# Kernel optimization log

Hardware: AMD Instinct MI355X
Metric: run time of the kernel (lower is better)

Reference implementation:

```python
import jax, jax.numpy as jnp
import numpy as np

B, N, C_IN, C_COORD, K = 2, 8192, 64, 3, 16
C_CAT = C_IN + C_COORD  # 67
HID1, HID2, C_OUT = 32, 64, 64


def setup_inputs() -> dict:
    key = jax.random.key(0)
    ks = jax.random.split(key, 10)
    s = 0.05
    return {
        "point_features": jax.random.normal(ks[0], (B, N, C_IN), jnp.float32),
        "coords": jax.random.uniform(ks[1], (B, N, C_COORD), jnp.float32),
        "w1": jax.random.normal(ks[2], (HID1, C_CAT), jnp.float32) * s,
        "b1": jax.random.normal(ks[3], (HID1,), jnp.float32) * s,
        "w2": jax.random.normal(ks[4], (HID2, HID1), jnp.float32) * s,
        "b2": jax.random.normal(ks[5], (HID2,), jnp.float32) * s,
        "w3": jax.random.normal(ks[6], (C_OUT, HID2), jnp.float32) * s,
        "b3": jax.random.normal(ks[7], (C_OUT,), jnp.float32) * s,
        "aggr_w": jax.random.normal(ks[8], (K,), jnp.float32) * s,
        "aggr_b": jax.random.normal(ks[9], (1,), jnp.float32) * s,
    }


def _knn_idx(coords):
    # squared pairwise distances: [B, N, N]
    sq = jnp.sum(coords * coords, axis=-1)
    d2 = sq[:, :, None] + sq[:, None, :] - 2.0 * jnp.einsum("bnc,bmc->bnm", coords, coords)
    # k smallest distances -> top_k of negated; self (d=0) lands at slot 0
    _, idx = jax.lax.top_k(-d2, K)  # [B, N, K]
    return idx


def reference(point_features, coords, w1, b1, w2, b2, w3, b3, aggr_w, aggr_b):
    idx = _knn_idx(coords)  # [B, N, K] int32
    feats = jnp.concatenate([point_features, coords], axis=-1)  # [B, N, C_CAT]
    # gather neighbor features -> [B, N, K, C_CAT]
    g = jax.vmap(lambda f, i: f[i])(feats, idx)
    # relative coords w.r.t. neighbor 0 (self)
    rel = g[..., -C_COORD:] - g[:, :, 0:1, -C_COORD:]
    g = jnp.concatenate([g[..., :C_IN], rel], axis=-1)
    # point pooling: max over K of raw input-feature channels
    y_pool = jnp.max(g[..., :C_IN], axis=2)  # [B, N, C_IN]
    # kernel MLP: stacked 1x1 convs, NO activations (act_func=None in source)
    h = jnp.einsum("bnkc,oc->bnko", g, w1) + b1
    h = jnp.einsum("bnkc,oc->bnko", h, w2) + b2
    h = jnp.einsum("bnkc,oc->bnko", h, w3) + b3  # [B, N, K, C_OUT]
    # attentive aggregation: Conv2d(K, 1, 1) over the K axis
    y_aggr = jnp.einsum("bnko,k->bno", h, aggr_w) + aggr_b  # [B, N, C_OUT]
    out_sum = jnp.sum(h, axis=2)  # [B, N, C_OUT]
    # concat order matches torch: (sum, pool, aggr), then permute -> B x N x C'
    return jnp.concatenate([out_sum, y_pool, y_aggr], axis=-1)
```

## Files before the change

### kernel.cpp

```cpp
#include <hip/hip_runtime.h>
#include <stdint.h>


typedef unsigned short u16;
typedef unsigned int   u32;
typedef unsigned long long u64;

#define NPTS  8192
#define KNB   16
#define SCAP  128
#define CAPA  512
#define QPW   8

__device__ __forceinline__ float bf2f(u16 u) {
    union { u32 i; float f; } v; v.i = ((u32)u) << 16; return v.f;
}
__device__ __forceinline__ u16 f2bf(float f) {
    u32 x = __float_as_uint(f);
    return (u16)((x + 0x7FFFu + ((x >> 16) & 1u)) >> 16);
}
__device__ __forceinline__ u32 fordkey(float f) {
    u32 u = __float_as_uint(f);
    return u ^ ((u32)((int)u >> 31) | 0x80000000u);
}
__device__ __forceinline__ u64 shflxor64(u64 v, int m) {
    int lo = __shfl_xor((int)(u32)v, m, 64);
    int hi = __shfl_xor((int)(u32)(v >> 32), m, 64);
    return ((u64)(u32)hi << 32) | (u32)lo;
}
__device__ __forceinline__ void wave_fence() {
    asm volatile("s_waitcnt lgkmcnt(0)" ::: "memory");
    __builtin_amdgcn_sched_barrier(0);
}
__device__ __forceinline__ float sq_np32(float x, float y, float z) {
    return __fadd_rn(__fadd_rn(__fmul_rn(x, x), __fmul_rn(y, y)), __fmul_rn(z, z));
}
__device__ __forceinline__ float d2_ref(float qx, float qy, float qz, float qsq,
                                        float x, float y, float z, float sq) {
    float dot = fmaf(z, qz, fmaf(y, qy, __fmul_rn(x, qx)));
    return __fsub_rn(__fadd_rn(qsq, sq), __fmul_rn(2.0f, dot));
}
__device__ __forceinline__ int cellof(float v) {
    int c = (int)floorf(v * 8.0f);
    return c < 0 ? 0 : (c > 7 ? 7 : c);
}

__global__ __launch_bounds__(256) void pack_count_kernel(
    const float* __restrict__ pf, const float* __restrict__ coords,
    u16* __restrict__ pfh, int* __restrict__ counts) {
    int gid = blockIdx.x * 256 + threadIdx.x;
    pfh[gid] = f2bf(pf[gid]);
    if (gid < 2 * NPTS) {
        float x = coords[gid * 3 + 0];
        float y = coords[gid * 3 + 1];
        float z = coords[gid * 3 + 2];
        int b = gid >> 13;
        int cell = (cellof(x) * 8 + cellof(y)) * 8 + cellof(z);
        atomicAdd(&counts[b * 512 + cell], 1);
    }
}

__global__ __launch_bounds__(512) void scan_kernel(
    const int* __restrict__ counts, int* __restrict__ cellStart,
    int* __restrict__ cellOffset) {
    __shared__ int s[512];
    int b = blockIdx.x, t = threadIdx.x;
    int myc = counts[b * 512 + t];
    s[t] = myc; __syncthreads();
#pragma unroll
    for (int off = 1; off < 512; off <<= 1) {
        int v = (t >= off) ? s[t - off] : 0; __syncthreads();
        s[t] += v; __syncthreads();
    }
    int excl = s[t] - myc;
    cellStart[b * 513 + t] = excl;
    cellOffset[b * 512 + t] = excl;
    if (t == 511) cellStart[b * 513 + 512] = s[511];
}

__global__ __launch_bounds__(256) void scatter_kernel(
    const float* __restrict__ coords, int* __restrict__ cellOffset,
    float4* __restrict__ spts, int* __restrict__ sidx) {
    int gid = blockIdx.x * 256 + threadIdx.x;
    float x = coords[gid * 3 + 0];
    float y = coords[gid * 3 + 1];
    float z = coords[gid * 3 + 2];
    int b = gid >> 13, i = gid & (NPTS - 1);
    int cell = (cellof(x) * 8 + cellof(y)) * 8 + cellof(z);
    int pos = atomicAdd(&cellOffset[b * 512 + cell], 1);
    spts[b * NPTS + pos] = make_float4(x, y, z, sq_np32(x, y, z));
    sidx[b * NPTS + pos] = i;
}

__device__ __forceinline__ void scan_seg(
    const float4* __restrict__ sp, const int* __restrict__ cs,
    u64* __restrict__ surv, int base, int z0, int z1,
    float qx, float qy, float qz, float qsq, float tau, int lane, int& cnt) {
    if (z0 > z1) return;
    int s = cs[base + z0], e = cs[base + z1 + 1];
    for (int i0 = s; i0 < e; i0 += 64) {
        int i = i0 + lane;
        bool valid = (i < e);
        int ii = valid ? i : (e - 1);
        float4 c = sp[ii];
        float d2 = d2_ref(qx, qy, qz, qsq, c.x, c.y, c.z, c.w);
        bool pass = valid && (d2 <= tau);
        u64 mask = __ballot(pass);
        if (pass) {
            int pre = __builtin_amdgcn_mbcnt_hi((u32)(mask >> 32),
                      __builtin_amdgcn_mbcnt_lo((u32)mask, 0));
            int pos = cnt + pre;
            if (pos < SCAP)
                surv[pos] = ((u64)fordkey(d2) << 32) | (u32)ii;
        }
        cnt += (int)__popcll(mask);
    }
}

__global__ __launch_bounds__(256, 6) void knn_kernel(
    const float4* __restrict__ spts, const int* __restrict__ sidx,
    const int* __restrict__ cellStart, int* __restrict__ idx_out) {
    __shared__ u64 allk_s[4][CAPA];
    __shared__ u64 surv_s[4][SCAP];

    const int lane = threadIdx.x & 63;
    const int wid  = threadIdx.x >> 6;
    u64* __restrict__ allk = allk_s[wid];
    u64* __restrict__ surv = surv_s[wid];

    const int blk  = blockIdx.x;
    const int sblk = (blk & 7) * 512 + (blk >> 3);
    const int p    = sblk * 4 + wid;
    const int b    = p >> 13;
    const float4* sp = spts + b * NPTS;
    const int*    si = sidx + b * NPTS;
    const int*    cs = cellStart + b * 513;

    float4 qc = sp[p & (NPTS - 1)];
    const float qx = qc.x, qy = qc.y, qz = qc.z, qsq = qc.w;
    int cqx = cellof(qx), cqy = cellof(qy), cqz = cellof(qz);

    const int ucqx = __builtin_amdgcn_readfirstlane(cqx);
    const int ucqy = __builtin_amdgcn_readfirstlane(cqy);
    const int ucqz = __builtin_amdgcn_readfirstlane(cqz);

    const int ax0 = max(ucqx - 1, 0), ax1 = min(ucqx + 1, 7);
    const int ay0 = max(ucqy - 1, 0), ay1 = min(ucqy + 1, 7);
    const int az0 = max(ucqz - 1, 0), az1 = min(ucqz + 1, 7);

    int segS[9], segE[9];
#pragma unroll
    for (int u = 0; u < 9; ++u) {
        int cx = ucqx - 1 + (u / 3);
        int cy = ucqy - 1 + (u % 3);
        bool ok = (cx >= 0) && (cx <= 7) && (cy >= 0) && (cy <= 7);
        if (ok) {
            int base = (cx * 8 + cy) * 8;
            segS[u] = cs[base + az0];
            segE[u] = cs[base + az1 + 1];
        } else {
            segS[u] = 0;
            segE[u] = 0;
        }
    }

    float dmin = 3.0e38f;
    int cnt0 = 0;
    bool ovf = false;
#pragma unroll
    for (int u = 0; u < 9; ++u) {
        int s = segS[u], e = segE[u];
#pragma unroll 1
        for (int i0 = s; i0 < e; i0 += 64) {
            int i = i0 + lane;
            bool valid = (i < e);
            int ii = valid ? i : (e - 1);
            float4 c = sp[ii];
            float d2 = d2_ref(qx, qy, qz, qsq, c.x, c.y, c.z, c.w);
            if (valid) dmin = fminf(dmin, d2);
            int add = (e - i0 < 64) ? (e - i0) : 64;
            if (!ovf && cnt0 + add <= CAPA) {
                if (valid)
                    allk[cnt0 + lane] = ((u64)fordkey(d2) << 32) | (u32)ii;
                cnt0 += add;
            } else {
                ovf = true;
            }
        }
    }
    wave_fence();

    {
        float v = dmin;
#pragma unroll
        for (int k = 2; k <= 64; k <<= 1) {
#pragma unroll
            for (int j2 = k >> 1; j2 >= 1; j2 >>= 1) {
                float o = __shfl_xor(v, j2, 64);
                bool lo = (lane & j2) == 0;
                bool up = (lane & k) == 0;
                float mn = fminf(v, o), mx = fmaxf(v, o);
                v = (lo == up) ? mn : mx;
            }
        }
        dmin = __shfl(v, 15, 64);
    }
    const float tau = dmin;

    float rr = sqrtf(tau + 1e-5f) + 1e-6f;
    int bx0 = max((int)floorf((qx - rr) * 8.0f), 0);
    int bx1 = min((int)floorf((qx + rr) * 8.0f), 7);
    int by0 = max((int)floorf((qy - rr) * 8.0f), 0);
    int by1 = min((int)floorf((qy + rr) * 8.0f), 7);
    int bz0 = max((int)floorf((qz - rr) * 8.0f), 0);
    int bz1 = min((int)floorf((qz + rr) * 8.0f), 7);
    int cnt = 0;
    if (!ovf) {
        const u32 taukey = fordkey(tau);
        for (int i0 = 0; i0 < cnt0; i0 += 64) {
            int i = i0 + lane;
            bool valid = (i < cnt0);
            u64 kk = valid ? allk[i] : ~0ull;
            bool pass = valid && ((u32)(kk >> 32) <= taukey);
            u64 mask = __ballot(pass);
            if (pass) {
                int pre = __builtin_amdgcn_mbcnt_hi((u32)(mask >> 32),
                          __builtin_amdgcn_mbcnt_lo((u32)mask, 0));
                int pos = cnt + pre;
                if (pos < SCAP) surv[pos] = kk;
            }
            cnt += (int)__popcll(mask);
        }
    }
#pragma unroll 1
    for (int cx = bx0; cx <= bx1; ++cx)
#pragma unroll 1
        for (int cy = by0; cy <= by1; ++cy) {
            int base = (cx * 8 + cy) * 8;
            bool colInA = !ovf && cx >= ax0 && cx <= ax1 &&
                          cy >= ay0 && cy <= ay1;
            if (colInA) {
                scan_seg(sp, cs, surv, base, bz0, min(az0 - 1, bz1),
                         qx, qy, qz, qsq, tau, lane, cnt);
                scan_seg(sp, cs, surv, base, max(az1 + 1, bz0), bz1,
                         qx, qy, qz, qsq, tau, lane, cnt);
            } else {
                scan_seg(sp, cs, surv, base, bz0, bz1,
                         qx, qy, qz, qsq, tau, lane, cnt);
            }
        }
    wave_fence();

    int myidx = 0;
    if (cnt <= 64) {
        u32 k32 = 0xffffffffu, p32 = 0xffffffffu;
        if (lane < cnt) {
            u64 kk = surv[lane];
            k32 = (u32)(kk >> 32);
            p32 = (u32)kk;
        }
#pragma unroll
        for (int k = 2; k <= 64; k <<= 1) {
#pragma unroll
            for (int j2 = k >> 1; j2 >= 1; j2 >>= 1) {
                u32 ok = (u32)__shfl_xor((int)k32, j2, 64);
                u32 op = (u32)__shfl_xor((int)p32, j2, 64);
                bool lo = (lane & j2) == 0;
                bool up = (lane & k) == 0;
                bool takemin = (lo == up);
                bool less = (ok < k32) || (ok == k32 && op < p32);
                bool take = (less == takemin);
                k32 = take ? ok : k32;
                p32 = take ? op : p32;
            }
        }
        myidx = (int)p32;
    } else {
        int cc = cnt > SCAP ? SCAP : cnt;
        u64 a0 = (lane < cc) ? surv[lane] : ~0ull;
        u64 a1 = (64 + lane < cc) ? surv[64 + lane] : ~0ull;
        if (a1 < a0) { u64 tmp = a0; a0 = a1; a1 = tmp; }
#pragma unroll 1
        for (int r = 0; r < 16; ++r) {
            u64 m = a0;
#pragma unroll
            for (int d = 1; d < 64; d <<= 1) {
                u64 o = shflxor64(m, d);
                m = (o < m) ? o : m;
            }
            if (a0 == m) { a0 = a1; a1 = ~0ull; }
            if (lane == r) myidx = (int)(u32)(m & 0xffffffffu);
        }
    }
    if (lane < KNB) {
        const int q = si[p & (NPTS - 1)];
        idx_out[((size_t)b * NPTS + q) * KNB + lane] =
            si[myidx & (NPTS - 1)];
    }
}

__global__ __launch_bounds__(64) void mlp_kernel(
    const u16* __restrict__ pfh, const float* __restrict__ coords,
    const float* __restrict__ w1, const float* __restrict__ b1,
    const float* __restrict__ w2, const float* __restrict__ b2,
    const float* __restrict__ w3, const float* __restrict__ b3,
    const float* __restrict__ aw, const float* __restrict__ ab,
    const int* __restrict__ knn_idx, const int* __restrict__ sidx,
    float* __restrict__ out) {

    __shared__ __attribute__((aligned(16))) float vbuf[2][68];
    __shared__ __attribute__((aligned(16))) float h1buf[2][36];

    const int lane = threadIdx.x;
    const int r    = lane & 31;
    const int vec  = lane >> 5;

    float w1r[68];
#pragma unroll
    for (int c = 0; c < 67; ++c) w1r[c] = w1[r * 67 + c];
    w1r[67] = 0.0f;
    float w2r[32];
    {
        const float4* p = (const float4*)(w2 + lane * 32);
#pragma unroll
        for (int c4 = 0; c4 < 8; ++c4) {
            float4 v = p[c4];
            w2r[c4 * 4 + 0] = v.x; w2r[c4 * 4 + 1] = v.y;
            w2r[c4 * 4 + 2] = v.z; w2r[c4 * 4 + 3] = v.w;
        }
    }
    float w3r[64];
    {
        const float4* p = (const float4*)(w3 + lane * 64);
#pragma unroll
        for (int c4 = 0; c4 < 16; ++c4) {
            float4 v = p[c4];
            w3r[c4 * 4 + 0] = v.x; w3r[c4 * 4 + 1] = v.y;
            w3r[c4 * 4 + 2] = v.z; w3r[c4 * 4 + 3] = v.w;
        }
    }
    float awr[16];
#pragma unroll
    for (int k = 0; k < 16; ++k) awr[k] = aw[k];
    float sa = 0.0f;
#pragma unroll
    for (int k = 0; k < 16; ++k) sa += awr[k];
    const float b1v = b1[r], b2v = b2[lane], b3v = b3[lane], abv = ab[0];
    const float c1 = (vec == 0) ? 16.0f : sa;

    const int sblk = (blockIdx.x & 7) * 256 + (blockIdx.x >> 3);

#pragma unroll 1
    for (int t = 0; t < QPW; ++t) {
        const int gp = sblk * QPW + t;
        const int b  = gp >> 13;
        const int q  = sidx[(size_t)b * NPTS + (gp & (NPTS - 1))];
        const int gq = b * NPTS + q;
        const u16*   pfb = pfh + (size_t)b * NPTS * 64;
        const float* cb  = coords + (size_t)b * NPTS * 3;

        int myi = knn_idx[(size_t)gq * KNB + (lane & 15)] & (NPTS - 1);

        float pool = -3.0e38f, G1 = 0.0f, Ga = 0.0f;
#pragma unroll
        for (int k = 0; k < 16; ++k) {
            int nk = __shfl(myi, k, 64);
            float v = bf2f(pfb[nk * 64 + lane]);
            pool = fmaxf(pool, v);
            G1 += v;
            Ga = fmaf(awr[k], v, Ga);
        }
        vbuf[0][lane] = G1;
        vbuf[1][lane] = Ga;

        if (lane < 48) {
            int j  = lane >> 4;
            int i0 = __shfl(myi, 0, 64);
            float rel  = cb[myi * 3 + j] - cb[i0 * 3 + j];
            float wrel = awr[lane & 15] * rel;
#pragma unroll
            for (int d = 1; d < 16; d <<= 1) {
                rel  += __shfl_xor(rel, d, 64);
                wrel += __shfl_xor(wrel, d, 64);
            }
            if ((lane & 15) == 0) { vbuf[0][64 + j] = rel; vbuf[1][64 + j] = wrel; }
        }
        if (lane == 0) { vbuf[0][67] = 0.0f; vbuf[1][67] = 0.0f; }
        __syncthreads();

        float acc = c1 * b1v;
        {
            const float4* vp = (const float4*)(&vbuf[vec][0]);
#pragma unroll
            for (int c4 = 0; c4 < 17; ++c4) {
                float4 g4 = vp[c4];
                acc = fmaf(g4.x, w1r[c4 * 4 + 0], acc);
                acc = fmaf(g4.y, w1r[c4 * 4 + 1], acc);
                acc = fmaf(g4.z, w1r[c4 * 4 + 2], acc);
                acc = fmaf(g4.w, w1r[c4 * 4 + 3], acc);
            }
        }
        h1buf[vec][r] = acc;
        __syncthreads();

        float a0 = 16.0f * b2v, a1 = sa * b2v;
        {
            const float4* p0 = (const float4*)(&h1buf[0][0]);
            const float4* p1 = (const float4*)(&h1buf[1][0]);
#pragma unroll
            for (int c4 = 0; c4 < 8; ++c4) {
                float4 x0 = p0[c4], x1 = p1[c4];
                a0 = fmaf(x0.x, w2r[c4 * 4 + 0], a0);
                a0 = fmaf(x0.y, w2r[c4 * 4 + 1], a0);
                a0 = fmaf(x0.z, w2r[c4 * 4 + 2], a0);
                a0 = fmaf(x0.w, w2r[c4 * 4 + 3], a0);
                a1 = fmaf(x1.x, w2r[c4 * 4 + 0], a1);
                a1 = fmaf(x1.y, w2r[c4 * 4 + 1], a1);
                a1 = fmaf(x1.z, w2r[c4 * 4 + 2], a1);
                a1 = fmaf(x1.w, w2r[c4 * 4 + 3], a1);
            }
        }
        __syncthreads();
        vbuf[0][lane] = a0;
        vbuf[1][lane] = a1;
        __syncthreads();

        float s1 = 16.0f * b3v, sA = sa * b3v;
        {
            const float4* p0 = (const float4*)(&vbuf[0][0]);
            const float4* p1 = (const float4*)(&vbuf[1][0]);
#pragma unroll
            for (int c4 = 0; c4 < 16; ++c4) {
                float4 x0 = p0[c4], x1 = p1[c4];
                s1 = fmaf(x0.x, w3r[c4 * 4 + 0], s1);
                s1 = fmaf(x0.y, w3r[c4 * 4 + 1], s1);
                s1 = fmaf(x0.z, w3r[c4 * 4 + 2], s1);
                s1 = fmaf(x0.w, w3r[c4 * 4 + 3], s1);
                sA = fmaf(x1.x, w3r[c4 * 4 + 0], sA);
                sA = fmaf(x1.y, w3r[c4 * 4 + 1], sA);
                sA = fmaf(x1.z, w3r[c4 * 4 + 2], sA);
                sA = fmaf(x1.w, w3r[c4 * 4 + 3], sA);
            }
        }
        float* op = out + (size_t)gq * 192;
        op[lane]       = s1;
        op[64 + lane]  = pool;
        op[128 + lane] = sA + abv;
        __syncthreads();
    }
}

extern "C" void kernel_launch(void* const* d_in, const int* in_sizes, int n_in,
                              void* d_out, int out_size, void* d_ws, size_t ws_size,
                              hipStream_t stream) {
    const float* pf     = (const float*)d_in[0];
    const float* coords = (const float*)d_in[1];
    const float* w1     = (const float*)d_in[2];
    const float* b1     = (const float*)d_in[3];
    const float* w2     = (const float*)d_in[4];
    const float* b2     = (const float*)d_in[5];
    const float* w3     = (const float*)d_in[6];
    const float* b3     = (const float*)d_in[7];
    const float* aw     = (const float*)d_in[8];
    const float* ab     = (const float*)d_in[9];

    char* ws = (char*)d_ws;
    int*    knn_idx    = (int*)ws;
    u16*    pfh        = (u16*)(ws + (1 << 20));
    float4* spts       = (float4*)(ws + (3 << 20));
    int*    sidx       = (int*)(ws + (3 << 20) + (256 << 10));
    int*    cellStart  = (int*)(ws + (3 << 20) + (320 << 10));
    int*    counts     = (int*)(ws + (3 << 20) + (328 << 10));
    int*    cellOffset = (int*)(ws + (3 << 20) + (336 << 10));
    float*  outp       = (float*)d_out;

    hipMemsetAsync(counts, 0, 2 * 512 * sizeof(int), stream);
    pack_count_kernel<<<4096, 256, 0, stream>>>(pf, coords, pfh, counts);
    scan_kernel<<<2, 512, 0, stream>>>(counts, cellStart, cellOffset);
    scatter_kernel<<<64, 256, 0, stream>>>(coords, cellOffset, spts, sidx);
    knn_kernel<<<4096, 256, 0, stream>>>(spts, sidx, cellStart, knn_idx);
    mlp_kernel<<<2048, 64, 0, stream>>>(pfh, coords, w1, b1, w2, b2, w3, b3,
                                        aw, ab, knn_idx, sidx, outp);
}
```

Before: 141.4 us.

## Process two KNN queries per wave with compact u32 candidate keys

Each wave now handles two query points, interleaving their candidate passes, bitonic threshold reductions and final sorts so the independent shuffle and load chains can overlap and hide latency. Candidate storage in LDS shrinks from 64-bit key/index pairs to 32-bit keys, with the index rebuilt from per-segment prefix offsets during filtering. Overflow is now decided up front from segment totals against a smaller capacity. The grid is halved to match. The trade-offs are higher register pressure and LDS use per wave, and a wave now waits on whichever of its two queries is slower.

```diff
diff --git a/kernel.cpp b/kernel.cpp
--- a/kernel.cpp
+++ b/kernel.cpp
@@ -9,7 +9,7 @@
 #define NPTS  8192
 #define KNB   16
 #define SCAP  128
-#define CAPA  512
+#define CAPA  480
 #define QPW   8
 
 __device__ __forceinline__ float bf2f(u16 u) {
@@ -117,59 +117,36 @@
     }
 }
 
-__global__ __launch_bounds__(256, 6) void knn_kernel(
-    const float4* __restrict__ spts, const int* __restrict__ sidx,
-    const int* __restrict__ cellStart, int* __restrict__ idx_out) {
-    __shared__ u64 allk_s[4][CAPA];
-    __shared__ u64 surv_s[4][SCAP];
-
-    const int lane = threadIdx.x & 63;
-    const int wid  = threadIdx.x >> 6;
-    u64* __restrict__ allk = allk_s[wid];
-    u64* __restrict__ surv = surv_s[wid];
-
-    const int blk  = blockIdx.x;
-    const int sblk = (blk & 7) * 512 + (blk >> 3);
-    const int p    = sblk * 4 + wid;
-    const int b    = p >> 13;
-    const float4* sp = spts + b * NPTS;
-    const int*    si = sidx + b * NPTS;
-    const int*    cs = cellStart + b * 513;
-
-    float4 qc = sp[p & (NPTS - 1)];
-    const float qx = qc.x, qy = qc.y, qz = qc.z, qsq = qc.w;
-    int cqx = cellof(qx), cqy = cellof(qy), cqz = cellof(qz);
-
-    const int ucqx = __builtin_amdgcn_readfirstlane(cqx);
-    const int ucqy = __builtin_amdgcn_readfirstlane(cqy);
-    const int ucqz = __builtin_amdgcn_readfirstlane(cqz);
-
-    const int ax0 = max(ucqx - 1, 0), ax1 = min(ucqx + 1, 7);
-    const int ay0 = max(ucqy - 1, 0), ay1 = min(ucqy + 1, 7);
-    const int az0 = max(ucqz - 1, 0), az1 = min(ucqz + 1, 7);
-
-    int segS[9], segE[9];
+__device__ __forceinline__ void segtab(
+    const int* __restrict__ cs, int ucx, int ucy, int az0, int az1,
+    int* segS, int* segE, int* pre, int& cnt0) {
+    int run = 0;
 #pragma unroll
     for (int u = 0; u < 9; ++u) {
-        int cx = ucqx - 1 + (u / 3);
-        int cy = ucqy - 1 + (u % 3);
+        int cx = ucx - 1 + (u / 3);
+        int cy = ucy - 1 + (u % 3);
         bool ok = (cx >= 0) && (cx <= 7) && (cy >= 0) && (cy <= 7);
+        int s = 0, e = 0;
         if (ok) {
             int base = (cx * 8 + cy) * 8;
-            segS[u] = cs[base + az0];
-            segE[u] = cs[base + az1 + 1];
-        } else {
-            segS[u] = 0;
-            segE[u] = 0;
-        }
-    }
-
-    float dmin = 3.0e38f;
-    int cnt0 = 0;
-    bool ovf = false;
+            s = cs[base + az0];
+            e = cs[base + az1 + 1];
+        }
+        segS[u] = s; segE[u] = e; pre[u] = run;
+        run += e - s;
+    }
+    cnt0 = run;
+}
+
+__device__ __forceinline__ void passA_one(
+    const float4* __restrict__ sp, u32* __restrict__ allk, int lane,
+    float qx, float qy, float qz, float qsq,
+    const int* segS, const int* segE, const int* pre, bool ovf,
+    float& dmin) {
 #pragma unroll
     for (int u = 0; u < 9; ++u) {
         int s = segS[u], e = segE[u];
+        int cb = pre[u] - s;
 #pragma unroll 1
         for (int i0 = s; i0 < e; i0 += 64) {
             int i = i0 + lane;
@@ -177,36 +154,46 @@
             int ii = valid ? i : (e - 1);
             float4 c = sp[ii];
             float d2 = d2_ref(qx, qy, qz, qsq, c.x, c.y, c.z, c.w);
-            if (valid) dmin = fminf(dmin, d2);
-            int add = (e - i0 < 64) ? (e - i0) : 64;
-            if (!ovf && cnt0 + add <= CAPA) {
-                if (valid)
-                    allk[cnt0 + lane] = ((u64)fordkey(d2) << 32) | (u32)ii;
-                cnt0 += add;
-            } else {
-                ovf = true;
-            }
-        }
-    }
-    wave_fence();
-
-    {
-        float v = dmin;
-#pragma unroll
-        for (int k = 2; k <= 64; k <<= 1) {
-#pragma unroll
-            for (int j2 = k >> 1; j2 >= 1; j2 >>= 1) {
-                float o = __shfl_xor(v, j2, 64);
-                bool lo = (lane & j2) == 0;
-                bool up = (lane & k) == 0;
-                float mn = fminf(v, o), mx = fmaxf(v, o);
-                v = (lo == up) ? mn : mx;
-            }
-        }
-        dmin = __shfl(v, 15, 64);
-    }
-    const float tau = dmin;
-
+            if (valid) {
+                dmin = fminf(dmin, d2);
+                if (!ovf) allk[cb + i] = fordkey(d2);
+            }
+        }
+    }
+}
+
+__device__ __forceinline__ int filter_lds(
+    const u32* __restrict__ allk, u64* __restrict__ surv,
+    const int* segS, const int* pre, int cnt0, u32 taukey, int lane) {
+    int cnt = 0;
+    for (int i0 = 0; i0 < cnt0; i0 += 64) {
+        int j = i0 + lane;
+        bool valid = (j < cnt0);
+        u32 kk = valid ? allk[j] : 0xffffffffu;
+        bool pass = valid && (kk <= taukey);
+        int off = segS[0];
+#pragma unroll
+        for (int u = 1; u < 9; ++u)
+            off = (j >= pre[u]) ? (segS[u] - pre[u]) : off;
+        int ii = j + off;
+        u64 mask = __ballot(pass);
+        if (pass) {
+            int pc = __builtin_amdgcn_mbcnt_hi((u32)(mask >> 32),
+                     __builtin_amdgcn_mbcnt_lo((u32)mask, 0));
+            int pos = cnt + pc;
+            if (pos < SCAP) surv[pos] = ((u64)kk << 32) | (u32)ii;
+        }
+        cnt += (int)__popcll(mask);
+    }
+    return cnt;
+}
+
+__device__ __forceinline__ void bbox_scan(
+    const float4* __restrict__ sp, const int* __restrict__ cs,
+    u64* __restrict__ surv,
+    float qx, float qy, float qz, float qsq, float tau,
+    int ax0, int ax1, int ay0, int ay1, int az0, int az1, bool ovf,
+    int lane, int& cnt) {
     float rr = sqrtf(tau + 1e-5f) + 1e-6f;
     int bx0 = max((int)floorf((qx - rr) * 8.0f), 0);
     int bx1 = min((int)floorf((qx + rr) * 8.0f), 7);
@@ -214,24 +201,6 @@
     int by1 = min((int)floorf((qy + rr) * 8.0f), 7);
     int bz0 = max((int)floorf((qz - rr) * 8.0f), 0);
     int bz1 = min((int)floorf((qz + rr) * 8.0f), 7);
-    int cnt = 0;
-    if (!ovf) {
-        const u32 taukey = fordkey(tau);
-        for (int i0 = 0; i0 < cnt0; i0 += 64) {
-            int i = i0 + lane;
-            bool valid = (i < cnt0);
-            u64 kk = valid ? allk[i] : ~0ull;
-            bool pass = valid && ((u32)(kk >> 32) <= taukey);
-            u64 mask = __ballot(pass);
-            if (pass) {
-                int pre = __builtin_amdgcn_mbcnt_hi((u32)(mask >> 32),
-                          __builtin_amdgcn_mbcnt_lo((u32)mask, 0));
-                int pos = cnt + pre;
-                if (pos < SCAP) surv[pos] = kk;
-            }
-            cnt += (int)__popcll(mask);
-        }
-    }
 #pragma unroll 1
     for (int cx = bx0; cx <= bx1; ++cx)
 #pragma unroll 1
@@ -249,8 +218,10 @@
                          qx, qy, qz, qsq, tau, lane, cnt);
             }
         }
-    wave_fence();
-
+}
+
+__device__ __forceinline__ int sel_one(const u64* __restrict__ surv,
+                                       int cnt, int lane) {
     int myidx = 0;
     if (cnt <= 64) {
         u32 k32 = 0xffffffffu, p32 = 0xffffffffu;
@@ -292,10 +263,132 @@
             if (lane == r) myidx = (int)(u32)(m & 0xffffffffu);
         }
     }
+    return myidx;
+}
+
+__global__ __launch_bounds__(256, 6) void knn_kernel(
+    const float4* __restrict__ spts, const int* __restrict__ sidx,
+    const int* __restrict__ cellStart, int* __restrict__ idx_out) {
+    __shared__ u32 allk_s[4][2][CAPA];
+    __shared__ u64 surv_s[4][2][SCAP];
+
+    const int lane = threadIdx.x & 63;
+    const int wid  = threadIdx.x >> 6;
+    u32* __restrict__ allkA = allk_s[wid][0];
+    u32* __restrict__ allkB = allk_s[wid][1];
+    u64* __restrict__ survA = surv_s[wid][0];
+    u64* __restrict__ survB = surv_s[wid][1];
+
+    const int blk  = blockIdx.x;
+    const int sblk = (blk & 7) * 256 + (blk >> 3);
+    const int pg   = sblk * 8 + wid * 2;
+    const int b    = pg >> 13;
+    const float4* sp = spts + b * NPTS;
+    const int*    si = sidx + b * NPTS;
+    const int*    cs = cellStart + b * 513;
+    const int plA = pg & (NPTS - 1);
+    const int plB = plA + 1;
+
+    float4 qcA = sp[plA];
+    float4 qcB = sp[plB];
+    const float qxA = qcA.x, qyA = qcA.y, qzA = qcA.z, qsA = qcA.w;
+    const float qxB = qcB.x, qyB = qcB.y, qzB = qcB.z, qsB = qcB.w;
+
+    const int uxA = __builtin_amdgcn_readfirstlane(cellof(qxA));
+    const int uyA = __builtin_amdgcn_readfirstlane(cellof(qyA));
+    const int uzA = __builtin_amdgcn_readfirstlane(cellof(qzA));
+    const int uxB = __builtin_amdgcn_readfirstlane(cellof(qxB));
+    const int uyB = __builtin_amdgcn_readfirstlane(cellof(qyB));
+    const int uzB = __builtin_amdgcn_readfirstlane(cellof(qzB));
+
+    const int axA0 = max(uxA - 1, 0), axA1 = min(uxA + 1, 7);
+    const int ayA0 = max(uyA - 1, 0), ayA1 = min(uyA + 1, 7);
+    const int azA0 = max(uzA - 1, 0), azA1 = min(uzA + 1, 7);
+    const int axB0 = max(uxB - 1, 0), axB1 = min(uxB + 1, 7);
+    const int ayB0 = max(uyB - 1, 0), ayB1 = min(uyB + 1, 7);
+    const int azB0 = max(uzB - 1, 0), azB1 = min(uzB + 1, 7);
+
+    int segSA[9], segEA[9], preA[9], cnt0A;
+    int segSB[9], segEB[9], preB[9], cnt0B;
+    segtab(cs, uxA, uyA, azA0, azA1, segSA, segEA, preA, cnt0A);
+    segtab(cs, uxB, uyB, azB0, azB1, segSB, segEB, preB, cnt0B);
+    const bool ovfA = cnt0A > CAPA;
+    const bool ovfB = cnt0B > CAPA;
+
+    float dminA = 3.0e38f, dminB = 3.0e38f;
+    passA_one(sp, allkA, lane, qxA, qyA, qzA, qsA, segSA, segEA, preA, ovfA, dminA);
+    passA_one(sp, allkB, lane, qxB, qyB, qzB, qsB, segSB, segEB, preB, ovfB, dminB);
+    wave_fence();
+
+    float vA = dminA, vB = dminB;
+#pragma unroll
+    for (int k = 2; k <= 64; k <<= 1) {
+#pragma unroll
+        for (int j2 = k >> 1; j2 >= 1; j2 >>= 1) {
+            float oA = __shfl_xor(vA, j2, 64);
+            float oB = __shfl_xor(vB, j2, 64);
+            bool lo = (lane & j2) == 0;
+            bool up = (lane & k) == 0;
+            bool tm = (lo == up);
+            float mnA = fminf(vA, oA), mxA = fmaxf(vA, oA);
+            float mnB = fminf(vB, oB), mxB = fmaxf(vB, oB);
+            vA = tm ? mnA : mxA;
+            vB = tm ? mnB : mxB;
+        }
+    }
+    const float tauA = __shfl(vA, 15, 64);
+    const float tauB = __shfl(vB, 15, 64);
+
+    int cntA = 0, cntB = 0;
+    if (!ovfA) cntA = filter_lds(allkA, survA, segSA, preA, cnt0A,
+                                 fordkey(tauA), lane);
+    if (!ovfB) cntB = filter_lds(allkB, survB, segSB, preB, cnt0B,
+                                 fordkey(tauB), lane);
+    bbox_scan(sp, cs, survA, qxA, qyA, qzA, qsA, tauA,
+              axA0, axA1, ayA0, ayA1, azA0, azA1, ovfA, lane, cntA);
+    bbox_scan(sp, cs, survB, qxB, qyB, qzB, qsB, tauB,
+              axB0, axB1, ayB0, ayB1, azB0, azB1, ovfB, lane, cntB);
+    wave_fence();
+
+    int myA, myB;
+    if (cntA <= 64 && cntB <= 64) {
+        u32 kA = 0xffffffffu, pA = 0xffffffffu;
+        u32 kB = 0xffffffffu, pB = 0xffffffffu;
+        if (lane < cntA) { u64 kk = survA[lane]; kA = (u32)(kk >> 32); pA = (u32)kk; }
+        if (lane < cntB) { u64 kk = survB[lane]; kB = (u32)(kk >> 32); pB = (u32)kk; }
+#pragma unroll
+        for (int k = 2; k <= 64; k <<= 1) {
+#pragma unroll
+            for (int j2 = k >> 1; j2 >= 1; j2 >>= 1) {
+                u32 okA = (u32)__shfl_xor((int)kA, j2, 64);
+                u32 opA = (u32)__shfl_xor((int)pA, j2, 64);
+                u32 okB = (u32)__shfl_xor((int)kB, j2, 64);
+                u32 opB = (u32)__shfl_xor((int)pB, j2, 64);
+                bool lo = (lane & j2) == 0;
+                bool up = (lane & k) == 0;
+                bool tm = (lo == up);
+                bool lessA = (okA < kA) || (okA == kA && opA < pA);
+                bool takeA = (lessA == tm);
+                kA = takeA ? okA : kA;
+                pA = takeA ? opA : pA;
+                bool lessB = (okB < kB) || (okB == kB && opB < pB);
+                bool takeB = (lessB == tm);
+                kB = takeB ? okB : kB;
+                pB = takeB ? opB : pB;
+            }
+        }
+        myA = (int)pA;
+        myB = (int)pB;
+    } else {
+        myA = sel_one(survA, cntA, lane);
+        myB = sel_one(survB, cntB, lane);
+    }
+
     if (lane < KNB) {
-        const int q = si[p & (NPTS - 1)];
-        idx_out[((size_t)b * NPTS + q) * KNB + lane] =
-            si[myidx & (NPTS - 1)];
+        const int qA = si[plA];
+        idx_out[((size_t)b * NPTS + qA) * KNB + lane] = si[myA & (NPTS - 1)];
+        const int qB = si[plB];
+        idx_out[((size_t)b * NPTS + qB) * KNB + lane] = si[myB & (NPTS - 1)];
     }
 }
 
@@ -478,7 +571,7 @@
     pack_count_kernel<<<4096, 256, 0, stream>>>(pf, coords, pfh, counts);
     scan_kernel<<<2, 512, 0, stream>>>(counts, cellStart, cellOffset);
     scatter_kernel<<<64, 256, 0, stream>>>(coords, cellOffset, spts, sidx);
-    knn_kernel<<<4096, 256, 0, stream>>>(spts, sidx, cellStart, knn_idx);
+    knn_kernel<<<2048, 256, 0, stream>>>(spts, sidx, cellStart, knn_idx);
     mlp_kernel<<<2048, 64, 0, stream>>>(pfh, coords, w1, b1, w2, b2, w3, b3,
                                         aw, ab, knn_idx, sidx, outp);
 }
```

Result: slower. 146.9 us (+3.8%).

## Fuse memset, count, scan and scatter into one cooperative grid-synced kernel

Applied to the files above, without the earlier changes.

Replaces the memset plus three small grid-build launches with a single cooperative kernel of 512 blocks that uses grid.sync between phases: zero counts, convert features to bf16 and count cells, scan per batch in two blocks, then scatter points into sorted cell order. This removes several launch gaps and the memset. In exchange it adds three grid-wide barriers, and the scan and scatter phases leave most blocks idle.

```diff
diff --git a/kernel.cpp b/kernel.cpp
--- a/kernel.cpp
+++ b/kernel.cpp
@@ -1,5 +1,8 @@
 #include <hip/hip_runtime.h>
+#include <hip/hip_cooperative_groups.h>
 #include <stdint.h>
+
+namespace cg = cooperative_groups;
 
 
 typedef unsigned short u16;
@@ -45,51 +48,69 @@
     return c < 0 ? 0 : (c > 7 ? 7 : c);
 }
 
-__global__ __launch_bounds__(256) void pack_count_kernel(
+__global__ __launch_bounds__(256) void build_kernel(
     const float* __restrict__ pf, const float* __restrict__ coords,
-    u16* __restrict__ pfh, int* __restrict__ counts) {
-    int gid = blockIdx.x * 256 + threadIdx.x;
-    pfh[gid] = f2bf(pf[gid]);
-    if (gid < 2 * NPTS) {
-        float x = coords[gid * 3 + 0];
-        float y = coords[gid * 3 + 1];
-        float z = coords[gid * 3 + 2];
-        int b = gid >> 13;
+    u16* __restrict__ pfh, int* __restrict__ counts,
+    int* __restrict__ cellStart, int* __restrict__ cellOffset,
+    float4* __restrict__ spts, int* __restrict__ sidx) {
+    cg::grid_group grid = cg::this_grid();
+    __shared__ int s[512];
+
+    const int t   = threadIdx.x;
+    const int blk = blockIdx.x;
+    const int g   = blk * 256 + t;
+
+    if (g < 1024) counts[g] = 0;
+    grid.sync();
+
+#pragma unroll
+    for (int j = 0; j < 8; ++j) {
+        int i = g + j * 131072;
+        pfh[i] = f2bf(pf[i]);
+    }
+    if (g < 2 * NPTS) {
+        float x = coords[g * 3 + 0];
+        float y = coords[g * 3 + 1];
+        float z = coords[g * 3 + 2];
+        int b = g >> 13;
         int cell = (cellof(x) * 8 + cellof(y)) * 8 + cellof(z);
         atomicAdd(&counts[b * 512 + cell], 1);
     }
-}
-
-__global__ __launch_bounds__(512) void scan_kernel(
-    const int* __restrict__ counts, int* __restrict__ cellStart,
-    int* __restrict__ cellOffset) {
-    __shared__ int s[512];
-    int b = blockIdx.x, t = threadIdx.x;
-    int myc = counts[b * 512 + t];
-    s[t] = myc; __syncthreads();
-#pragma unroll
-    for (int off = 1; off < 512; off <<= 1) {
-        int v = (t >= off) ? s[t - off] : 0; __syncthreads();
-        s[t] += v; __syncthreads();
-    }
-    int excl = s[t] - myc;
-    cellStart[b * 513 + t] = excl;
-    cellOffset[b * 512 + t] = excl;
-    if (t == 511) cellStart[b * 513 + 512] = s[511];
-}
-
-__global__ __launch_bounds__(256) void scatter_kernel(
-    const float* __restrict__ coords, int* __restrict__ cellOffset,
-    float4* __restrict__ spts, int* __restrict__ sidx) {
-    int gid = blockIdx.x * 256 + threadIdx.x;
-    float x = coords[gid * 3 + 0];
-    float y = coords[gid * 3 + 1];
-    float z = coords[gid * 3 + 2];
-    int b = gid >> 13, i = gid & (NPTS - 1);
-    int cell = (cellof(x) * 8 + cellof(y)) * 8 + cellof(z);
-    int pos = atomicAdd(&cellOffset[b * 512 + cell], 1);
-    spts[b * NPTS + pos] = make_float4(x, y, z, sq_np32(x, y, z));
-    sidx[b * NPTS + pos] = i;
+    grid.sync();
+
+    if (blk < 2) {
+        const int b = blk;
+        int c0 = counts[b * 512 + t];
+        int c1 = counts[b * 512 + t + 256];
+        s[t] = c0; s[t + 256] = c1;
+        __syncthreads();
+#pragma unroll
+        for (int off = 1; off < 512; off <<= 1) {
+            int v0 = (t >= off) ? s[t - off] : 0;
+            int v1 = (t + 256 >= off) ? s[t + 256 - off] : 0;
+            __syncthreads();
+            s[t] += v0; s[t + 256] += v1;
+            __syncthreads();
+        }
+        int e0 = s[t] - c0, e1 = s[t + 256] - c1;
+        cellStart[b * 513 + t]        = e0;
+        cellStart[b * 513 + t + 256]  = e1;
+        cellOffset[b * 512 + t]       = e0;
+        cellOffset[b * 512 + t + 256] = e1;
+        if (t == 255) cellStart[b * 513 + 512] = s[511];
+    }
+    grid.sync();
+
+    if (g < 2 * NPTS) {
+        float x = coords[g * 3 + 0];
+        float y = coords[g * 3 + 1];
+        float z = coords[g * 3 + 2];
+        int b = g >> 13, i = g & (NPTS - 1);
+        int cell = (cellof(x) * 8 + cellof(y)) * 8 + cellof(z);
+        int pos = atomicAdd(&cellOffset[b * 512 + cell], 1);
+        spts[b * NPTS + pos] = make_float4(x, y, z, sq_np32(x, y, z));
+        sidx[b * NPTS + pos] = i;
+    }
 }
 
 __device__ __forceinline__ void scan_seg(
@@ -474,10 +495,12 @@
     int*    cellOffset = (int*)(ws + (3 << 20) + (336 << 10));
     float*  outp       = (float*)d_out;
 
-    hipMemsetAsync(counts, 0, 2 * 512 * sizeof(int), stream);
-    pack_count_kernel<<<4096, 256, 0, stream>>>(pf, coords, pfh, counts);
-    scan_kernel<<<2, 512, 0, stream>>>(counts, cellStart, cellOffset);
-    scatter_kernel<<<64, 256, 0, stream>>>(coords, cellOffset, spts, sidx);
+    void* bargs[] = {
+        (void*)&pf, (void*)&coords, (void*)&pfh, (void*)&counts,
+        (void*)&cellStart, (void*)&cellOffset, (void*)&spts, (void*)&sidx
+    };
+    hipLaunchCooperativeKernel((void*)build_kernel, dim3(512), dim3(256),
+                               bargs, 0, stream);
     knn_kernel<<<4096, 256, 0, stream>>>(spts, sidx, cellStart, knn_idx);
     mlp_kernel<<<2048, 64, 0, stream>>>(pfh, coords, w1, b1, w2, b2, w3, b3,
                                         aw, ab, knn_idx, sidx, outp);
```

New measurement: 303.1 us. 114% more time.
